# Kernel tuning notes

Measured on AMD Instinct MI355X. Metric: run time of the kernel, lower is better.

Reference implementation:

```python
import jax, jax.numpy as jnp
import numpy as np

TAU = 100.0
DT = 20.0
ALPHA = DT / TAU  # 0.2, fixed buffer (train_alpha=False)


def setup_inputs() -> dict:
    key = jax.random.key(0)
    ks = jax.random.split(key, 12)
    T, B, I, H = 64, 32, 128, 256

    def lin(kw, out_f, in_f):
        bound = 1.0 / np.sqrt(in_f)
        kw1, kw2 = jax.random.split(kw)
        w = jax.random.uniform(kw1, (out_f, in_f), jnp.float32, -bound, bound)
        b = jax.random.uniform(kw2, (out_f,), jnp.float32, -bound, bound)
        return w, b

    w_i2h, b_i2h = lin(ks[0], H, I)
    w_h2h, b_h2h = lin(ks[1], H, H)
    w_i2c, b_i2c = lin(ks[2], H, I)
    w_c2c, b_c2c = lin(ks[3], H, H)
    w_c2t, b_c2t = lin(ks[4], H * H, H)
    x = jax.random.normal(ks[5], (T, B, I), jnp.float32)
    return {
        "input": x,
        "w_i2h": w_i2h, "b_i2h": b_i2h,
        "w_h2h": w_h2h, "b_h2h": b_h2h,
        "w_i2c": w_i2c, "b_i2c": b_i2c,
        "w_c2c": w_c2c, "b_c2c": b_c2c,
        "w_c2t": w_c2t, "b_c2t": b_c2t,
        "num_steps": 1,
    }


def reference(input, w_i2h, b_i2h, w_h2h, b_h2h, w_i2c, b_i2c,
              w_c2c, b_c2c, w_c2t, b_c2t, num_steps):
    H = w_i2h.shape[0]
    B = input.shape[1]
    a = jnp.float32(ALPHA)

    def recurrence(x, hidden, context):
        input_proj = x @ w_i2h.T + b_i2h                      # [B,H]
        tm = (context @ w_c2t.T + b_c2t).reshape(B, H, H)     # per-sample hypernet matrix
        transformed = jnp.einsum('bij,bj->bi', tm, input_proj)
        h_new = jax.nn.relu(context + transformed + hidden @ w_h2h.T + b_h2h)
        hidden = hidden * (1 - a) + h_new * a
        context_new = jax.nn.relu(context @ w_c2c.T + b_c2c + x @ w_i2c.T + b_i2c)
        context = context * (1 - a) + context_new * a
        hidden = transformed  # NOTE: faithful to source, overwrites leaky update
        return hidden, context

    def step(carry, x):
        hidden, context = carry
        for _ in range(num_steps):
            hidden, context = recurrence(x, hidden, context)
        return (hidden, context), hidden

    h0 = jnp.zeros((B, H), input.dtype)
    c0 = jnp.zeros((B, H), input.dtype)
    (hidden, context), output = jax.lax.scan(step, (h0, c0), input)
    return output, hidden, context
```

## Files before the change

### kernel.cpp

```cpp
#include <hip/hip_runtime.h>

#define TT 64
#define BB 32
#define II 128
#define HH 256
#define MM (TT*BB)

typedef __bf16  bf16x8  __attribute__((ext_vector_type(8)));
typedef float   f32x16  __attribute__((ext_vector_type(16)));
typedef _Float16 half2v __attribute__((ext_vector_type(2)));

__device__ __forceinline__ float bf2f(unsigned short u) {
    union { unsigned int i; float f; } v; v.i = ((unsigned int)u) << 16; return v.f;
}
__device__ __forceinline__ unsigned short f2bf(float f) {
    union { float f; unsigned int i; } v; v.f = f;
    unsigned int r = v.i + 0x7fffu + ((v.i >> 16) & 1u);
    return (unsigned short)(r >> 16);
}

struct F8 { float v[8]; };
__device__ __forceinline__ F8 load8(const void* base, int idx, int isf32) {
    F8 r;
    if (isf32) {
        const float4* p = (const float4*)((const float*)base + idx);
        float4 a = p[0], b = p[1];
        r.v[0]=a.x; r.v[1]=a.y; r.v[2]=a.z; r.v[3]=a.w;
        r.v[4]=b.x; r.v[5]=b.y; r.v[6]=b.z; r.v[7]=b.w;
    } else {
        uint4 u = *(const uint4*)((const unsigned short*)base + idx);
        const unsigned short* p = (const unsigned short*)&u;
#pragma unroll
        for (int j = 0; j < 8; ++j) r.v[j] = bf2f(p[j]);
    }
    return r;
}
__device__ __forceinline__ float load1(const void* base, int idx, int isf32) {
    return isf32 ? ((const float*)base)[idx]
                 : bf2f(((const unsigned short*)base)[idx]);
}

__device__ __forceinline__ float fdot2f(half2v a, half2v b, float c) {
#if __has_builtin(__builtin_amdgcn_fdot2)
    return __builtin_amdgcn_fdot2(a, b, c, false);
#else
    return c + (float)a.x*(float)b.x + (float)a.y*(float)b.y;
#endif
}

__global__ __launch_bounds__(256) void k0_sniff(
    const unsigned short* __restrict__ x, int* __restrict__ flag)
{
    __shared__ int cnt;
    if (threadIdx.x == 0) cnt = 0;
    __syncthreads();
    int c = 0;
    for (int i = threadIdx.x; i < 8192; i += 256) {
        unsigned int e = (x[i] >> 7) & 0xFFu;
        if (e >= 0xC0u) ++c;
    }
    atomicAdd(&cnt, c);
    __syncthreads();
    if (threadIdx.x == 0) flag[0] = (cnt > 16) ? 1 : 0;
}

__global__ __launch_bounds__(256) void k1_proj(
    const void* __restrict__ x,
    const void* __restrict__ w_i2h,
    const void* __restrict__ b_i2h,
    const void* __restrict__ w_i2c,
    const void* __restrict__ b_i2c,
    const int* __restrict__ flagp,
    unsigned short* __restrict__ ip,
    float* __restrict__ cin)
{
    const int isf32 = *flagp;
    const int tid = threadIdx.x;
    const int h = tid;
    const int mbase = blockIdx.x * 32;
    __shared__ __align__(16) _Float16 xs[32][II];

    half2v w1[II/2], w2[II/2];
#pragma unroll
    for (int c8 = 0; c8 < II/8; ++c8) {
        F8 f1 = load8(w_i2h, h*II + c8*8, isf32);
        F8 f2 = load8(w_i2c, h*II + c8*8, isf32);
#pragma unroll
        for (int j = 0; j < 4; ++j) {
            half2v a; a.x = (_Float16)f1.v[2*j]; a.y = (_Float16)f1.v[2*j+1];
            half2v b; b.x = (_Float16)f2.v[2*j]; b.y = (_Float16)f2.v[2*j+1];
            w1[c8*4 + j] = a;
            w2[c8*4 + j] = b;
        }
    }
    const float bb1 = load1(b_i2h, h, isf32);
    const float bb2 = load1(b_i2c, h, isf32);

    for (int u = tid; u < 32*II; u += 256)
        xs[u >> 7][u & (II-1)] = (_Float16)load1(x, (mbase + (u >> 7))*II + (u & (II-1)), isf32);
    __syncthreads();

    for (int mm = 0; mm < 32; ++mm) {
        const half2v* xv = (const half2v*)xs[mm];
        float a0=0,a1=0,a2=0,a3=0, c0=0,c1=0,c2=0,c3=0;
#pragma unroll
        for (int r = 0; r < II/2; r += 4) {
            half2v x0 = xv[r], x1 = xv[r+1], x2 = xv[r+2], x3 = xv[r+3];
            a0 = fdot2f(w1[r],   x0, a0);
            a1 = fdot2f(w1[r+1], x1, a1);
            a2 = fdot2f(w1[r+2], x2, a2);
            a3 = fdot2f(w1[r+3], x3, a3);
            c0 = fdot2f(w2[r],   x0, c0);
            c1 = fdot2f(w2[r+1], x1, c1);
            c2 = fdot2f(w2[r+2], x2, c2);
            c3 = fdot2f(w2[r+3], x3, c3);
        }
        ip[(mbase+mm)*HH + h]  = f2bf(((a0+a1)+(a2+a3)) + bb1);
        cin[(mbase+mm)*HH + h] = ((c0+c1)+(c2+c3)) + bb2;
    }
}

__global__ __launch_bounds__(256) void k2_ctx(
    const void* __restrict__ w_c2c,
    const void* __restrict__ b_c2c,
    const float* __restrict__ cin,
    const int* __restrict__ ns_ptr,
    const int* __restrict__ flagp,
    unsigned short* __restrict__ ctx_hist,
    void* __restrict__ out_base)
{
    const int isf32 = *flagp;
    const int b = blockIdx.x;
    const int h = threadIdx.x;
    const int ns = max(1, *ns_ptr);

    __shared__ __align__(16) _Float16 cs[2][HH];

    half2v w[HH/2];
#pragma unroll
    for (int c8 = 0; c8 < HH/8; ++c8) {
        F8 f = load8(w_c2c, h*HH + c8*8, isf32);
#pragma unroll
        for (int j = 0; j < 4; ++j) {
            half2v hv;
            hv.x = (_Float16)f.v[2*j];
            hv.y = (_Float16)f.v[2*j+1];
            w[c8*4 + j] = hv;
        }
    }
    const float bcc = load1(b_c2c, h, isf32);
    float ctxv = 0.0f;
    cs[0][h] = (_Float16)0.0f;
    __syncthreads();
    int cur = 0;

    for (int t = 0; t < TT; ++t) {
        const float cinv = cin[(t*BB + b)*HH + h];
        for (int s = 0; s < ns; ++s) {
            if (s == ns-1) ctx_hist[(t*BB + b)*HH + h] = f2bf(ctxv);
            float p0=0,p1=0,p2=0,p3=0;
            const float4* cp4 = (const float4*)cs[cur];
#pragma unroll
            for (int r4 = 0; r4 < HH/8; ++r4) {
                float4 blob = cp4[r4];
                const half2v* c2 = (const half2v*)&blob;
                p0 = fdot2f(w[r4*4+0], c2[0], p0);
                p1 = fdot2f(w[r4*4+1], c2[1], p1);
                p2 = fdot2f(w[r4*4+2], c2[2], p2);
                p3 = fdot2f(w[r4*4+3], c2[3], p3);
            }
            float cnew = fmaxf(((p0+p1)+(p2+p3)) + bcc + cinv, 0.0f);
            ctxv = 0.8f*ctxv + 0.2f*cnew;
            cs[cur^1][h] = (_Float16)ctxv;
            cur ^= 1;
            __syncthreads();
        }
    }
    const int cofs = MM*HH + BB*HH + b*HH + h;
    if (isf32) ((float*)out_base)[cofs] = ctxv;
    else       ((unsigned short*)out_base)[cofs] = f2bf(ctxv);
}

__global__ __launch_bounds__(512, 2) void k3_main(
    const unsigned short* __restrict__ ctx_hist,
    const void* __restrict__ wc,
    const void* __restrict__ bc,
    const unsigned short* __restrict__ ip,
    const int* __restrict__ flagp,
    void* __restrict__ out)
{
    extern __shared__ __align__(16) unsigned char lds[];
    unsigned short* Bs = (unsigned short*)lds;
    unsigned short* As = (unsigned short*)(lds + 131072);
    float*          TMf = (float*)(lds + 131072);

    const int isf32 = *flagp;
    const int tid  = threadIdx.x;
    const int lane = tid & 63;
    const int wave = tid >> 6;
    const int i    = blockIdx.x;
    const int mh   = wave & 3;
    const int jh   = wave >> 2;
    const int l31  = lane & 31;
    const int lhi  = lane >> 5;

    const int eml = tid >> 4;
    const int ecs = tid & 15;

    float bcp[16];
    {
        F8 f0 = load8(bc, i*HH + ecs*16,     isf32);
        F8 f1 = load8(bc, i*HH + ecs*16 + 8, isf32);
#pragma unroll
        for (int j = 0; j < 8; ++j) { bcp[j] = f0.v[j]; bcp[8+j] = f1.v[j]; }
    }

#pragma unroll
    for (int p = 0; p < 16; ++p) {
        int u = tid + p*512;
        int row = u >> 5, cu = u & 31;
        F8 f = load8(wc, (i*HH + row)*HH + cu*8, isf32);
        unsigned short tmp[8];
#pragma unroll
        for (int j = 0; j < 8; ++j) tmp[j] = f2bf(f.v[j]);
        *(uint4*)(Bs + row*256 + ((cu ^ (row & 7)) << 3)) = *(const uint4*)tmp;
    }

    for (int mc = 0; mc < 8; ++mc) {
        const int m0 = mc * 256;

        f32x16 acc[2][4];
#pragma unroll
        for (int a = 0; a < 2; ++a)
#pragma unroll
            for (int n = 0; n < 4; ++n)
#pragma unroll
                for (int r = 0; r < 16; ++r) acc[a][n][r] = 0.0f;

#pragma unroll
        for (int kc = 0; kc < 4; ++kc) {
            const int k0 = kc * 64;
#pragma unroll
            for (int p = 0; p < 4; ++p) {
                int u = tid + p*512;
                int row = u >> 3, cu = u & 7;
                uint4 v = *(const uint4*)(ctx_hist + (m0 + row)*HH + k0 + cu*8);
                *(uint4*)(As + row*64 + ((cu ^ (row & 7)) << 3)) = v;
            }
            __syncthreads();
#pragma unroll
            for (int ks = 0; ks < 4; ++ks) {
                const int cA = ks*2 + lhi;
                const int ra0 = mh*64 + l31;
                const int ra1 = ra0 + 32;
                bf16x8 a0 = *(const bf16x8*)(As + ra0*64 + ((cA ^ (ra0 & 7)) << 3));
                bf16x8 a1 = *(const bf16x8*)(As + ra1*64 + ((cA ^ (ra1 & 7)) << 3));
                const int cB = kc*8 + ks*2 + lhi;
                const int rb0 = jh*128 +       l31;
                const int rb1 = jh*128 + 32  + l31;
                const int rb2 = jh*128 + 64  + l31;
                const int rb3 = jh*128 + 96  + l31;
                bf16x8 b0 = *(const bf16x8*)(Bs + rb0*256 + ((cB ^ (rb0 & 7)) << 3));
                bf16x8 b1 = *(const bf16x8*)(Bs + rb1*256 + ((cB ^ (rb1 & 7)) << 3));
                bf16x8 b2 = *(const bf16x8*)(Bs + rb2*256 + ((cB ^ (rb2 & 7)) << 3));
                bf16x8 b3 = *(const bf16x8*)(Bs + rb3*256 + ((cB ^ (rb3 & 7)) << 3));
                acc[0][0] = __builtin_amdgcn_mfma_f32_32x32x16_bf16(a0, b0, acc[0][0], 0, 0, 0);
                acc[0][1] = __builtin_amdgcn_mfma_f32_32x32x16_bf16(a0, b1, acc[0][1], 0, 0, 0);
                acc[0][2] = __builtin_amdgcn_mfma_f32_32x32x16_bf16(a0, b2, acc[0][2], 0, 0, 0);
                acc[0][3] = __builtin_amdgcn_mfma_f32_32x32x16_bf16(a0, b3, acc[0][3], 0, 0, 0);
                acc[1][0] = __builtin_amdgcn_mfma_f32_32x32x16_bf16(a1, b0, acc[1][0], 0, 0, 0);
                acc[1][1] = __builtin_amdgcn_mfma_f32_32x32x16_bf16(a1, b1, acc[1][1], 0, 0, 0);
                acc[1][2] = __builtin_amdgcn_mfma_f32_32x32x16_bf16(a1, b2, acc[1][2], 0, 0, 0);
                acc[1][3] = __builtin_amdgcn_mfma_f32_32x32x16_bf16(a1, b3, acc[1][3], 0, 0, 0);
            }
            __syncthreads();
        }

#pragma unroll
        for (int ch = 0; ch < 8; ++ch) {
            if (mh == (ch >> 1)) {
                const int a = ch & 1;
#pragma unroll
                for (int n = 0; n < 4; ++n) {
                    const int j  = jh*128 + n*32 + l31;
                    const int ju = j >> 2, jo = j & 3;
#pragma unroll
                    for (int r = 0; r < 16; ++r) {
                        const int row16 = (r & 3) + 8*(r >> 2) + 4*lhi;
                        TMf[row16*256 + ((ju ^ (row16 & 7)) << 2) + jo] = acc[a][n][r];
                    }
                }
            }
            __syncthreads();
            {
                const int g = m0 + ch*32 + eml;
                float ipf[16];
                {
                    uint4 u0 = *(const uint4*)(ip + g*HH + ecs*16);
                    uint4 u1 = *(const uint4*)(ip + g*HH + ecs*16 + 8);
                    const unsigned short* p0 = (const unsigned short*)&u0;
                    const unsigned short* p1 = (const unsigned short*)&u1;
#pragma unroll
                    for (int j = 0; j < 8; ++j) { ipf[j] = bf2f(p0[j]); ipf[8+j] = bf2f(p1[j]); }
                }
                const float4* TM4 = (const float4*)TMf;
                float s = 0.0f;
#pragma unroll
                for (int u = 0; u < 4; ++u) {
                    float4 t = TM4[eml*64 + ((ecs*4 + u) ^ (eml & 7))];
                    s = fmaf(t.x + bcp[u*4+0], ipf[u*4+0], s);
                    s = fmaf(t.y + bcp[u*4+1], ipf[u*4+1], s);
                    s = fmaf(t.z + bcp[u*4+2], ipf[u*4+2], s);
                    s = fmaf(t.w + bcp[u*4+3], ipf[u*4+3], s);
                }
                s += __shfl_xor(s, 1);
                s += __shfl_xor(s, 2);
                s += __shfl_xor(s, 4);
                s += __shfl_xor(s, 8);
                if (ecs == 0) {
                    if (isf32) {
                        float* o = (float*)out;
                        o[g*HH + i] = s;
                        if (g >= MM - BB) o[MM*HH + (g - (MM-BB))*HH + i] = s;
                    } else {
                        unsigned short* o = (unsigned short*)out;
                        const unsigned short v = f2bf(s);
                        o[g*HH + i] = v;
                        if (g >= MM - BB) o[MM*HH + (g - (MM-BB))*HH + i] = v;
                    }
                }
            }
            __syncthreads();
        }
    }
}

extern "C" void kernel_launch(void* const* d_in, const int* in_sizes, int n_in,
                              void* d_out, int out_size, void* d_ws, size_t ws_size,
                              hipStream_t stream) {
    const void* x     = d_in[0];
    const void* w_i2h = d_in[1];
    const void* b_i2h = d_in[2];
    const void* w_i2c = d_in[5];
    const void* b_i2c = d_in[6];
    const void* w_c2c = d_in[7];
    const void* b_c2c = d_in[8];
    const void* w_c2t = d_in[9];
    const void* b_c2t = d_in[10];
    const int* ns     = (const int*)d_in[11];

    unsigned short* ip  = (unsigned short*)d_ws;
    unsigned short* ch  = (unsigned short*)((char*)d_ws + (size_t)MM*HH*2);
    float* cin          = (float*)((char*)d_ws + (size_t)MM*HH*4);
    int* flag           = (int*)((char*)d_ws + (size_t)MM*HH*8);

    static bool attr_done = false;
    (void)hipFuncSetAttribute((const void*)k3_main,
                              hipFuncAttributeMaxDynamicSharedMemorySize, 163840);
    (void)attr_done;

    k0_sniff<<<1, 256, 0, stream>>>((const unsigned short*)x, flag);
    k1_proj<<<64, 256, 0, stream>>>(x, w_i2h, b_i2h, w_i2c, b_i2c, flag, ip, cin);
    k2_ctx<<<BB, 256, 0, stream>>>(w_c2c, b_c2c, cin, ns, flag, ch, d_out);
    k3_main<<<256, 512, 163840, stream>>>(ch, w_c2t, b_c2t, ip, flag, d_out);
}
```

Baseline: 339.8 us.

## Fuse hypernet contraction into MFMA epilogue and register-prefetch context tiles

The k3 main loop now swaps the MFMA operand roles so each wave holds a 64(j) x 128(m) accumulator tile. The bias-add and dot product with the input projection are done directly from accumulator registers, with a single cross-wave reduction through LDS. This replaces the eight-chunk LDS staging of the transformed matrix and its many barriers. It also prefetches the next context-history tile into registers while the current one is consumed, overlapping global loads with MFMA work. The costs are higher register pressure and uncoalesced 8-byte global reads of ip per lane.

```diff
diff --git a/kernel.cpp b/kernel.cpp
--- a/kernel.cpp
+++ b/kernel.cpp
@@ -190,30 +190,35 @@
     void* __restrict__ out)
 {
     extern __shared__ __align__(16) unsigned char lds[];
-    unsigned short* Bs = (unsigned short*)lds;
+    unsigned short* Ws = (unsigned short*)lds;
     unsigned short* As = (unsigned short*)(lds + 131072);
-    float*          TMf = (float*)(lds + 131072);
+    float*          Ps = (float*)(lds + 131072);
 
     const int isf32 = *flagp;
     const int tid  = threadIdx.x;
     const int lane = tid & 63;
     const int wave = tid >> 6;
     const int i    = blockIdx.x;
-    const int mh   = wave & 3;
-    const int jh   = wave >> 2;
+    const int jq   = wave & 3;
+    const int mh   = wave >> 1 >> 1;
     const int l31  = lane & 31;
     const int lhi  = lane >> 5;
 
-    const int eml = tid >> 4;
-    const int ecs = tid & 15;
-
-    float bcp[16];
-    {
-        F8 f0 = load8(bc, i*HH + ecs*16,     isf32);
-        F8 f1 = load8(bc, i*HH + ecs*16 + 8, isf32);
-#pragma unroll
-        for (int j = 0; j < 8; ++j) { bcp[j] = f0.v[j]; bcp[8+j] = f1.v[j]; }
-    }
+    float bcv[2][4][4];
+#pragma unroll
+    for (int a = 0; a < 2; ++a)
+#pragma unroll
+        for (int g = 0; g < 4; ++g) {
+            const int j0 = i*HH + jq*64 + a*32 + lhi*4 + g*8;
+            if (isf32) {
+                float4 t = *(const float4*)((const float*)bc + j0);
+                bcv[a][g][0]=t.x; bcv[a][g][1]=t.y; bcv[a][g][2]=t.z; bcv[a][g][3]=t.w;
+            } else {
+                ushort4 t = *(const ushort4*)((const unsigned short*)bc + j0);
+                bcv[a][g][0]=bf2f(t.x); bcv[a][g][1]=bf2f(t.y);
+                bcv[a][g][2]=bf2f(t.z); bcv[a][g][3]=bf2f(t.w);
+            }
+        }
 
 #pragma unroll
     for (int p = 0; p < 16; ++p) {
@@ -223,7 +228,14 @@
         unsigned short tmp[8];
 #pragma unroll
         for (int j = 0; j < 8; ++j) tmp[j] = f2bf(f.v[j]);
-        *(uint4*)(Bs + row*256 + ((cu ^ (row & 7)) << 3)) = *(const uint4*)tmp;
+        *(uint4*)(Ws + row*256 + ((cu ^ (row & 7)) << 3)) = *(const uint4*)tmp;
+    }
+
+    uint4 gbuf[4];
+#pragma unroll
+    for (int p = 0; p < 4; ++p) {
+        const int u = tid + p*512;
+        gbuf[p] = *(const uint4*)(ctx_hist + (u >> 3)*HH + (u & 7)*8);
     }
 
     for (int mc = 0; mc < 8; ++mc) {
@@ -239,98 +251,89 @@
 
 #pragma unroll
         for (int kc = 0; kc < 4; ++kc) {
-            const int k0 = kc * 64;
+            __syncthreads();
 #pragma unroll
             for (int p = 0; p < 4; ++p) {
-                int u = tid + p*512;
-                int row = u >> 3, cu = u & 7;
-                uint4 v = *(const uint4*)(ctx_hist + (m0 + row)*HH + k0 + cu*8);
-                *(uint4*)(As + row*64 + ((cu ^ (row & 7)) << 3)) = v;
+                const int u = tid + p*512;
+                const int row = u >> 3, cu = u & 7;
+                *(uint4*)(As + row*64 + ((cu ^ (row & 7)) << 3)) = gbuf[p];
+            }
+            {
+                const int nc  = (mc*4 + kc + 1) & 31;
+                const int nm0 = (nc >> 2) * 256, nk0 = (nc & 3) * 64;
+#pragma unroll
+                for (int p = 0; p < 4; ++p) {
+                    const int u = tid + p*512;
+                    gbuf[p] = *(const uint4*)(ctx_hist + (nm0 + (u >> 3))*HH + nk0 + (u & 7)*8);
+                }
             }
             __syncthreads();
 #pragma unroll
             for (int ks = 0; ks < 4; ++ks) {
-                const int cA = ks*2 + lhi;
-                const int ra0 = mh*64 + l31;
-                const int ra1 = ra0 + 32;
-                bf16x8 a0 = *(const bf16x8*)(As + ra0*64 + ((cA ^ (ra0 & 7)) << 3));
-                bf16x8 a1 = *(const bf16x8*)(As + ra1*64 + ((cA ^ (ra1 & 7)) << 3));
-                const int cB = kc*8 + ks*2 + lhi;
-                const int rb0 = jh*128 +       l31;
-                const int rb1 = jh*128 + 32  + l31;
-                const int rb2 = jh*128 + 64  + l31;
-                const int rb3 = jh*128 + 96  + l31;
-                bf16x8 b0 = *(const bf16x8*)(Bs + rb0*256 + ((cB ^ (rb0 & 7)) << 3));
-                bf16x8 b1 = *(const bf16x8*)(Bs + rb1*256 + ((cB ^ (rb1 & 7)) << 3));
-                bf16x8 b2 = *(const bf16x8*)(Bs + rb2*256 + ((cB ^ (rb2 & 7)) << 3));
-                bf16x8 b3 = *(const bf16x8*)(Bs + rb3*256 + ((cB ^ (rb3 & 7)) << 3));
-                acc[0][0] = __builtin_amdgcn_mfma_f32_32x32x16_bf16(a0, b0, acc[0][0], 0, 0, 0);
-                acc[0][1] = __builtin_amdgcn_mfma_f32_32x32x16_bf16(a0, b1, acc[0][1], 0, 0, 0);
-                acc[0][2] = __builtin_amdgcn_mfma_f32_32x32x16_bf16(a0, b2, acc[0][2], 0, 0, 0);
-                acc[0][3] = __builtin_amdgcn_mfma_f32_32x32x16_bf16(a0, b3, acc[0][3], 0, 0, 0);
-                acc[1][0] = __builtin_amdgcn_mfma_f32_32x32x16_bf16(a1, b0, acc[1][0], 0, 0, 0);
-                acc[1][1] = __builtin_amdgcn_mfma_f32_32x32x16_bf16(a1, b1, acc[1][1], 0, 0, 0);
-                acc[1][2] = __builtin_amdgcn_mfma_f32_32x32x16_bf16(a1, b2, acc[1][2], 0, 0, 0);
-                acc[1][3] = __builtin_amdgcn_mfma_f32_32x32x16_bf16(a1, b3, acc[1][3], 0, 0, 0);
-            }
-            __syncthreads();
-        }
-
-#pragma unroll
-        for (int ch = 0; ch < 8; ++ch) {
-            if (mh == (ch >> 1)) {
-                const int a = ch & 1;
-#pragma unroll
-                for (int n = 0; n < 4; ++n) {
-                    const int j  = jh*128 + n*32 + l31;
-                    const int ju = j >> 2, jo = j & 3;
-#pragma unroll
-                    for (int r = 0; r < 16; ++r) {
-                        const int row16 = (r & 3) + 8*(r >> 2) + 4*lhi;
-                        TMf[row16*256 + ((ju ^ (row16 & 7)) << 2) + jo] = acc[a][n][r];
-                    }
+                const int cB  = kc*8 + ks*2 + lhi;
+                const int rj0 = jq*64 + l31;
+                const int rj1 = rj0 + 32;
+                bf16x8 w0 = *(const bf16x8*)(Ws + rj0*256 + ((cB ^ (rj0 & 7)) << 3));
+                bf16x8 w1 = *(const bf16x8*)(Ws + rj1*256 + ((cB ^ (rj1 & 7)) << 3));
+                const int cA  = ks*2 + lhi;
+                const int rm0 = mh*128 +      l31;
+                const int rm1 = rm0 + 32;
+                const int rm2 = rm0 + 64;
+                const int rm3 = rm0 + 96;
+                bf16x8 c0 = *(const bf16x8*)(As + rm0*64 + ((cA ^ (rm0 & 7)) << 3));
+                bf16x8 c1 = *(const bf16x8*)(As + rm1*64 + ((cA ^ (rm1 & 7)) << 3));
+                bf16x8 c2 = *(const bf16x8*)(As + rm2*64 + ((cA ^ (rm2 & 7)) << 3));
+                bf16x8 c3 = *(const bf16x8*)(As + rm3*64 + ((cA ^ (rm3 & 7)) << 3));
+                acc[0][0] = __builtin_amdgcn_mfma_f32_32x32x16_bf16(w0, c0, acc[0][0], 0, 0, 0);
+                acc[0][1] = __builtin_amdgcn_mfma_f32_32x32x16_bf16(w0, c1, acc[0][1], 0, 0, 0);
+                acc[0][2] = __builtin_amdgcn_mfma_f32_32x32x16_bf16(w0, c2, acc[0][2], 0, 0, 0);
+                acc[0][3] = __builtin_amdgcn_mfma_f32_32x32x16_bf16(w0, c3, acc[0][3], 0, 0, 0);
+                acc[1][0] = __builtin_amdgcn_mfma_f32_32x32x16_bf16(w1, c0, acc[1][0], 0, 0, 0);
+                acc[1][1] = __builtin_amdgcn_mfma_f32_32x32x16_bf16(w1, c1, acc[1][1], 0, 0, 0);
+                acc[1][2] = __builtin_amdgcn_mfma_f32_32x32x16_bf16(w1, c2, acc[1][2], 0, 0, 0);
+                acc[1][3] = __builtin_amdgcn_mfma_f32_32x32x16_bf16(w1, c3, acc[1][3], 0, 0, 0);
+            }
+        }
+
+        float sv[4];
+#pragma unroll
+        for (int n = 0; n < 4; ++n) {
+            const unsigned short* iprow =
+                ip + (m0 + mh*128 + n*32 + l31)*HH + jq*64 + lhi*4;
+            float s = 0.0f;
+#pragma unroll
+            for (int a = 0; a < 2; ++a)
+#pragma unroll
+                for (int g = 0; g < 4; ++g) {
+                    ushort4 t = *(const ushort4*)(iprow + a*32 + g*8);
+                    s = fmaf(acc[a][n][g*4+0] + bcv[a][g][0], bf2f(t.x), s);
+                    s = fmaf(acc[a][n][g*4+1] + bcv[a][g][1], bf2f(t.y), s);
+                    s = fmaf(acc[a][n][g*4+2] + bcv[a][g][2], bf2f(t.z), s);
+                    s = fmaf(acc[a][n][g*4+3] + bcv[a][g][3], bf2f(t.w), s);
                 }
-            }
-            __syncthreads();
-            {
-                const int g = m0 + ch*32 + eml;
-                float ipf[16];
-                {
-                    uint4 u0 = *(const uint4*)(ip + g*HH + ecs*16);
-                    uint4 u1 = *(const uint4*)(ip + g*HH + ecs*16 + 8);
-                    const unsigned short* p0 = (const unsigned short*)&u0;
-                    const unsigned short* p1 = (const unsigned short*)&u1;
-#pragma unroll
-                    for (int j = 0; j < 8; ++j) { ipf[j] = bf2f(p0[j]); ipf[8+j] = bf2f(p1[j]); }
-                }
-                const float4* TM4 = (const float4*)TMf;
-                float s = 0.0f;
-#pragma unroll
-                for (int u = 0; u < 4; ++u) {
-                    float4 t = TM4[eml*64 + ((ecs*4 + u) ^ (eml & 7))];
-                    s = fmaf(t.x + bcp[u*4+0], ipf[u*4+0], s);
-                    s = fmaf(t.y + bcp[u*4+1], ipf[u*4+1], s);
-                    s = fmaf(t.z + bcp[u*4+2], ipf[u*4+2], s);
-                    s = fmaf(t.w + bcp[u*4+3], ipf[u*4+3], s);
-                }
-                s += __shfl_xor(s, 1);
-                s += __shfl_xor(s, 2);
-                s += __shfl_xor(s, 4);
-                s += __shfl_xor(s, 8);
-                if (ecs == 0) {
-                    if (isf32) {
-                        float* o = (float*)out;
-                        o[g*HH + i] = s;
-                        if (g >= MM - BB) o[MM*HH + (g - (MM-BB))*HH + i] = s;
-                    } else {
-                        unsigned short* o = (unsigned short*)out;
-                        const unsigned short v = f2bf(s);
-                        o[g*HH + i] = v;
-                        if (g >= MM - BB) o[MM*HH + (g - (MM-BB))*HH + i] = v;
-                    }
-                }
-            }
-            __syncthreads();
+            s += __shfl_xor(s, 32);
+            sv[n] = s;
+        }
+        __syncthreads();
+        if (lhi == 0) {
+#pragma unroll
+            for (int n = 0; n < 4; ++n)
+                Ps[jq*256 + mh*128 + n*32 + l31] = sv[n];
+        }
+        __syncthreads();
+        if (tid < 256) {
+            const float r = Ps[tid] + Ps[256+tid] + Ps[512+tid] + Ps[768+tid];
+            const int gr = m0 + tid;
+            if (isf32) {
+                float* o = (float*)out;
+                o[gr*HH + i] = r;
+                if (gr >= MM - BB) o[MM*HH + (gr - (MM-BB))*HH + i] = r;
+            } else {
+                unsigned short* o = (unsigned short*)out;
+                const unsigned short v = f2bf(r);
+                o[gr*HH + i] = v;
+                if (gr >= MM - BB) o[MM*HH + (gr - (MM-BB))*HH + i] = v;
+            }
         }
     }
 }
@@ -354,10 +357,8 @@
     float* cin          = (float*)((char*)d_ws + (size_t)MM*HH*4);
     int* flag           = (int*)((char*)d_ws + (size_t)MM*HH*8);
 
-    static bool attr_done = false;
     (void)hipFuncSetAttribute((const void*)k3_main,
                               hipFuncAttributeMaxDynamicSharedMemorySize, 163840);
-    (void)attr_done;
 
     k0_sniff<<<1, 256, 0, stream>>>((const unsigned short*)x, flag);
     k1_proj<<<64, 256, 0, stream>>>(x, w_i2h, b_i2h, w_i2c, b_i2c, flag, ip, cin);
```

After: 370.9 us. 1.09x slower.
